# Kernel optimization log

Measured on AMD Instinct MI355X. Metric: run time of the kernel, lower is better.

The kernel has to match this reference:

```python
import jax, jax.numpy as jnp
import numpy as np

H = 512   # lstm_hidden_size
B = 64    # batch
S = 256   # seqlen


def setup_inputs() -> dict:
    key = jax.random.key(0)
    ks = jax.random.split(key, 6)
    scale = 1.0 / np.sqrt(H)  # PyTorch LSTM default init range
    return {
        "x": jax.random.normal(ks[0], (B, S, 2 * H), dtype=jnp.float32),
        "hi": jax.random.normal(ks[1], (B, S, 2 * H), dtype=jnp.float32),
        "W_ih": jax.random.uniform(ks[2], (4 * H, 5 * H), minval=-scale, maxval=scale, dtype=jnp.float32),
        "W_hh": jax.random.uniform(ks[3], (4 * H, H), minval=-scale, maxval=scale, dtype=jnp.float32),
        "b_ih": jax.random.uniform(ks[4], (4 * H,), minval=-scale, maxval=scale, dtype=jnp.float32),
        "b_hh": jax.random.uniform(ks[5], (4 * H,), minval=-scale, maxval=scale, dtype=jnp.float32),
    }


def _forward(x, hi, W_ih, W_hh, b_ih, b_hh):
    h_dim = W_hh.shape[1]
    bias = b_ih + b_hh
    xc = jnp.concatenate([x, hi], axis=-1)          # [B, S, 4H]
    xc = jnp.transpose(xc, (1, 0, 2))               # [S, B, 4H]
    batch = xc.shape[1]

    def cell(hc, inp_b):
        # inp_b: [5H]; PyTorch LSTM treats the batch dim as seq (batch_first=False quirk)
        h, c = hc
        gates = inp_b @ W_ih.T + h @ W_hh.T + bias  # [4H]
        i_g, f_g, g_g, o_g = jnp.split(gates, 4)
        i_g = jax.nn.sigmoid(i_g)
        f_g = jax.nn.sigmoid(f_g)
        g_g = jnp.tanh(g_g)
        o_g = jax.nn.sigmoid(o_g)
        c = f_g * c + i_g * g_g
        h = o_g * jnp.tanh(c)
        return (h, c), h

    def step(carry, x_i):
        out_prev, h, c = carry                      # out_prev: [B, H]
        inp = jnp.concatenate([x_i, out_prev], axis=-1)  # [B, 5H]
        (h, c), outs = jax.lax.scan(cell, (h, c), inp)    # scan over batch dim
        return (outs, h, c), outs

    init = (jnp.zeros((batch, h_dim), x.dtype),
            jnp.zeros((h_dim,), x.dtype),
            jnp.zeros((h_dim,), x.dtype))
    _, all_out = jax.lax.scan(step, init, xc)       # [S, B, H]
    return jnp.transpose(all_out, (1, 0, 2))        # [B, S, H]


def reference(x, hi, W_ih, W_hh, b_ih, b_hh):
    # Dropout layers are identity in eval mode.
    return _forward(x, hi, W_ih, W_hh, b_ih, b_hh)
```

## Files before the change

### kernel.cpp

```cpp
#include <hip/hip_runtime.h>

typedef _Float16 f16;
typedef _Float16 f16x2 __attribute__((ext_vector_type(2)));
typedef _Float16 f16x4 __attribute__((ext_vector_type(4)));
typedef _Float16 f16x8 __attribute__((ext_vector_type(8)));
typedef float f32x4 __attribute__((ext_vector_type(4)));
typedef unsigned int u32;
typedef unsigned int u32x4 __attribute__((ext_vector_type(4)));
typedef unsigned long long ull;

#define HD 512
#define T_TOT 16384
#define RING 128
#define NWG 16
#define NTH 512

static const size_t O_XC    = 0;
static const size_t O_W1    = 67108864;
static const size_t O_WHH   = 75497472;
static const size_t O_W2    = 77594624;
static const size_t O_G     = 79691776;
static const size_t O_RINGL = 213909504;
static const size_t O_RINGG = 214171648;
static const size_t O_ELECT = 214433792;

__device__ __forceinline__ float dot2f(f16x2 a, f16x2 b, float c) {
#if __has_builtin(__builtin_amdgcn_fdot2)
    return __builtin_amdgcn_fdot2(a, b, c, false);
#else
    return fmaf((float)a[0], (float)b[0], fmaf((float)a[1], (float)b[1], c));
#endif
}
__device__ __forceinline__ f16x2 bcf(u32 u) { return __builtin_bit_cast(f16x2, u); }

__device__ __forceinline__ float sigf(float x) { return 1.0f / (1.0f + __expf(-x)); }
__device__ __forceinline__ float tanhfast(float x) { return 1.0f - 2.0f / (__expf(2.0f * x) + 1.0f); }

__device__ __forceinline__ ull ld_a64(const ull* p) {
    return __hip_atomic_load(p, __ATOMIC_RELAXED, __HIP_MEMORY_SCOPE_AGENT);
}
__device__ __forceinline__ void st_a64(ull* p, ull v) {
    __hip_atomic_store(p, v, __ATOMIC_RELAXED, __HIP_MEMORY_SCOPE_AGENT);
}
__device__ __forceinline__ void ld4_sc0(const ull* p, ull& a, ull& b, ull& c, ull& d) {
    asm volatile("global_load_dwordx2 %0, %4, off sc0\n\t"
                 "global_load_dwordx2 %1, %4, off offset:8 sc0\n\t"
                 "global_load_dwordx2 %2, %4, off offset:16 sc0\n\t"
                 "global_load_dwordx2 %3, %4, off offset:24 sc0\n\t"
                 "s_waitcnt vmcnt(0)"
                 : "=&v"(a), "=&v"(b), "=&v"(c), "=&v"(d) : "v"(p) : "memory");
}
__device__ __forceinline__ void st1_sc0(ull* p, ull v) {
    asm volatile("global_store_dwordx2 %0, %1, off sc0" :: "v"(p), "v"(v) : "memory");
}

__global__ __launch_bounds__(256) void conv_xc(const float* __restrict__ x,
                                               const float* __restrict__ hi,
                                               f16* __restrict__ xc) {
    int gid = blockIdx.x * 256 + threadIdx.x;
    int t = gid >> 9;
    int k = (gid & 511) << 2;
    int b = t & 63, s = t >> 6;
    const float* src = (k < 1024) ? (x  + ((size_t)((b << 8) + s) << 10) + k)
                                  : (hi + ((size_t)((b << 8) + s) << 10) + (k - 1024));
    float4 v = *reinterpret_cast<const float4*>(src);
    f16x4 o = { (_Float16)v.x, (_Float16)v.y, (_Float16)v.z, (_Float16)v.w };
    *reinterpret_cast<f16x4*>(xc + ((size_t)t << 11) + k) = o;
}

__global__ __launch_bounds__(256) void conv_w1(const float* __restrict__ wih,
                                               f16* __restrict__ w1) {
    int gid = blockIdx.x * 256 + threadIdx.x;
    int j = gid >> 9;
    int k = (gid & 511) << 2;
    float4 v = *reinterpret_cast<const float4*>(wih + (size_t)j * 2560 + k);
    f16x4 o = { (_Float16)v.x, (_Float16)v.y, (_Float16)v.z, (_Float16)v.w };
    *reinterpret_cast<f16x4*>(w1 + ((size_t)j << 11) + k) = o;
}

__global__ __launch_bounds__(256) void conv_wc(const float* __restrict__ whh,
                                               const float* __restrict__ wih,
                                               f16* __restrict__ whhf,
                                               f16* __restrict__ w2f) {
    int gid = blockIdx.x * 256 + threadIdx.x;
    int j = gid >> 7;
    int k = (gid & 127) << 2;
    float4 a = *reinterpret_cast<const float4*>(whh + (size_t)j * 512 + k);
    f16x4 oa = { (_Float16)a.x, (_Float16)a.y, (_Float16)a.z, (_Float16)a.w };
    *reinterpret_cast<f16x4*>(whhf + ((size_t)j << 9) + k) = oa;
    float4 bv = *reinterpret_cast<const float4*>(wih + (size_t)j * 2560 + 2048 + k);
    f16x4 ob = { (_Float16)bv.x, (_Float16)bv.y, (_Float16)bv.z, (_Float16)bv.w };
    *reinterpret_cast<f16x4*>(w2f + ((size_t)j << 9) + k) = ob;
}

__global__ __launch_bounds__(256) void gemm_pre(const f16* __restrict__ XC,
                                                const f16* __restrict__ W1,
                                                const float* __restrict__ b_ih,
                                                const float* __restrict__ b_hh,
                                                float* __restrict__ G) {
    int w = threadIdx.x >> 6, l = threadIdx.x & 63;
    int R0 = blockIdx.y * 128 + (w >> 1) * 64;
    int C0 = blockIdx.x * 128 + (w & 1) * 64;
    int lr = l & 15, kb = l >> 4;
    f32x4 acc[4][4] = {};
    const f16* Abase = XC + (size_t)(R0 + lr) * 2048 + kb * 8;
    const f16* Bbase = W1 + (size_t)(C0 + lr) * 2048 + kb * 8;
    for (int kk = 0; kk < 2048; kk += 32) {
        f16x8 av[4], bv[4];
#pragma unroll
        for (int i = 0; i < 4; i++)
            av[i] = *reinterpret_cast<const f16x8*>(Abase + (size_t)(i * 16) * 2048 + kk);
#pragma unroll
        for (int i = 0; i < 4; i++)
            bv[i] = *reinterpret_cast<const f16x8*>(Bbase + (size_t)(i * 16) * 2048 + kk);
#pragma unroll
        for (int fr = 0; fr < 4; fr++)
#pragma unroll
            for (int fc = 0; fc < 4; fc++)
                acc[fr][fc] = __builtin_amdgcn_mfma_f32_16x16x32_f16(av[fr], bv[fc], acc[fr][fc], 0, 0, 0);
    }
#pragma unroll
    for (int fc = 0; fc < 4; fc++) {
        int col = C0 + fc * 16 + lr;
        float bias = b_ih[col] + b_hh[col];
#pragma unroll
        for (int fr = 0; fr < 4; fr++) {
#pragma unroll
            for (int r = 0; r < 4; r++) {
                int row = R0 + fr * 16 + kb * 4 + r;
                G[(size_t)row * 2048 + col] = acc[fr][fc][r] + bias;
            }
        }
    }
}

template <int COOP>
__global__ __launch_bounds__(NTH, 1) void lstm_chain_t(const float* __restrict__ G,
                                                       const f16* __restrict__ Whhf,
                                                       const f16* __restrict__ W2f,
                                                       ull* __restrict__ ringL,
                                                       ull* __restrict__ ringG,
                                                       int* __restrict__ elect,
                                                       float* __restrict__ out) {
    __shared__ u32 hist[96][256];
    __shared__ __align__(16) float part[2][32][4];
    __shared__ int s_slot;

    const int tid = threadIdx.x;
    int wg;
    if (COOP) {
        if (tid == 0) {
            int xcc = 0;
            asm volatile("s_getreg_b32 %0, hwreg(HW_REG_XCC_ID, 0, 32)" : "=s"(xcc));
            xcc &= 7;
            int s = atomicAdd(&elect[xcc], 1);
            if (s == 15) atomicCAS(&elect[8], 0, xcc + 1);
            int w;
            do {
                w = __hip_atomic_load(&elect[8], __ATOMIC_RELAXED, __HIP_MEMORY_SCOPE_AGENT);
            } while (w == 0);
            s_slot = (w - 1 == xcc && s < NWG) ? s : -1;
        }
        __syncthreads();
        wg = s_slot;
        if (wg < 0) return;
    } else {
        wg = blockIdx.x;
    }

    const int wv = tid >> 6, l = tid & 63;
    const int g = wv & 3, uh = (wv >> 2) & 1;
    const int rr = ((l & 1) << 3) | ((l & 2) << 1) | ((l & 4) >> 1) | ((l & 8) >> 3);
    const int row0 = g * 512 + wg * 32 + uh * 16;
    const int growD = row0 + rr;

    for (int i = tid; i < 4096; i += NTH)
        reinterpret_cast<u32x4*>(hist)[i] = (u32x4){0u, 0u, 0u, 0u};

    u32x4 w1v[16], w2v[16];
    {
        const f16* a0 = Whhf + (size_t)row0 * 512 + 8 * l;
        const f16* a1 = a0 + 4 * 512;
        const f16* a2 = a0 + 8 * 512;
        const f16* a3 = a0 + 12 * 512;
        asm volatile(
            "global_load_dwordx4 %0, %16, off\n\t"
            "global_load_dwordx4 %1, %16, off offset:1024\n\t"
            "global_load_dwordx4 %2, %16, off offset:2048\n\t"
            "global_load_dwordx4 %3, %16, off offset:3072\n\t"
            "global_load_dwordx4 %4, %17, off\n\t"
            "global_load_dwordx4 %5, %17, off offset:1024\n\t"
            "global_load_dwordx4 %6, %17, off offset:2048\n\t"
            "global_load_dwordx4 %7, %17, off offset:3072\n\t"
            "global_load_dwordx4 %8, %18, off\n\t"
            "global_load_dwordx4 %9, %18, off offset:1024\n\t"
            "global_load_dwordx4 %10, %18, off offset:2048\n\t"
            "global_load_dwordx4 %11, %18, off offset:3072\n\t"
            "global_load_dwordx4 %12, %19, off\n\t"
            "global_load_dwordx4 %13, %19, off offset:1024\n\t"
            "global_load_dwordx4 %14, %19, off offset:2048\n\t"
            "global_load_dwordx4 %15, %19, off offset:3072\n\t"
            "s_waitcnt vmcnt(0)"
            : "=&v"(w1v[0]), "=&v"(w1v[1]), "=&v"(w1v[2]), "=&v"(w1v[3]),
              "=&v"(w1v[4]), "=&v"(w1v[5]), "=&v"(w1v[6]), "=&v"(w1v[7]),
              "=&v"(w1v[8]), "=&v"(w1v[9]), "=&v"(w1v[10]), "=&v"(w1v[11]),
              "=&v"(w1v[12]), "=&v"(w1v[13]), "=&v"(w1v[14]), "=&v"(w1v[15])
            : "v"(a0), "v"(a1), "v"(a2), "v"(a3) : "memory");
        const f16* b0p = W2f + (size_t)row0 * 512 + 8 * l;
        const f16* b1p = b0p + 4 * 512;
        const f16* b2p = b0p + 8 * 512;
        const f16* b3p = b0p + 12 * 512;
        asm volatile(
            "global_load_dwordx4 %0, %16, off\n\t"
            "global_load_dwordx4 %1, %16, off offset:1024\n\t"
            "global_load_dwordx4 %2, %16, off offset:2048\n\t"
            "global_load_dwordx4 %3, %16, off offset:3072\n\t"
            "global_load_dwordx4 %4, %17, off\n\t"
            "global_load_dwordx4 %5, %17, off offset:1024\n\t"
            "global_load_dwordx4 %6, %17, off offset:2048\n\t"
            "global_load_dwordx4 %7, %17, off offset:3072\n\t"
            "global_load_dwordx4 %8, %18, off\n\t"
            "global_load_dwordx4 %9, %18, off offset:1024\n\t"
            "global_load_dwordx4 %10, %18, off offset:2048\n\t"
            "global_load_dwordx4 %11, %18, off offset:3072\n\t"
            "global_load_dwordx4 %12, %19, off\n\t"
            "global_load_dwordx4 %13, %19, off offset:1024\n\t"
            "global_load_dwordx4 %14, %19, off offset:2048\n\t"
            "global_load_dwordx4 %15, %19, off offset:3072\n\t"
            "s_waitcnt vmcnt(0)"
            : "=&v"(w2v[0]), "=&v"(w2v[1]), "=&v"(w2v[2]), "=&v"(w2v[3]),
              "=&v"(w2v[4]), "=&v"(w2v[5]), "=&v"(w2v[6]), "=&v"(w2v[7]),
              "=&v"(w2v[8]), "=&v"(w2v[9]), "=&v"(w2v[10]), "=&v"(w2v[11]),
              "=&v"(w2v[12]), "=&v"(w2v[13]), "=&v"(w2v[14]), "=&v"(w2v[15])
            : "v"(b0p), "v"(b1p), "v"(b2p), "v"(b3p) : "memory");
    }

    float cst = 0.0f;
    float gv = (l < 16) ? G[growD] : 0.0f;
    bool fb = (COOP == 0);
    __syncthreads();

    for (int t = 0; t < T_TOT; t++) {
        const int buf = t & 1;

        float ac[16];
#pragma unroll
        for (int r = 0; r < 16; r++) ac[r] = 0.0f;
        {
            u32x4 hv = *reinterpret_cast<const u32x4*>(&hist[t & 63][4 * l]);
            f16x2 h0 = bcf(hv.x), h1 = bcf(hv.y), h2 = bcf(hv.z), h3 = bcf(hv.w);
#pragma unroll
            for (int r = 0; r < 16; r++) {
                ac[r] = dot2f(bcf(w2v[r].x), h0, ac[r]);
                ac[r] = dot2f(bcf(w2v[r].y), h1, ac[r]);
                ac[r] = dot2f(bcf(w2v[r].z), h2, ac[r]);
                ac[r] = dot2f(bcf(w2v[r].w), h3, ac[r]);
            }
        }
        int tn = (t + 1 < T_TOT) ? t + 1 : t;
        float gnext = (l < 16) ? G[(size_t)tn * 2048 + growD] : 0.0f;

        u32x4 hB;
        if (wv == 0) {
            __builtin_amdgcn_s_setprio(1);
            const size_t soff = (size_t)((t - 1) & (RING - 1)) * 256 + 4 * l;
            const u32 want = (u32)t;
            ull b0 = 0, b1 = 0, b2 = 0, b3 = 0;
            bool got = false;
            if (!fb) {
                int tries = 0;
                while (!got && tries < 512) {
                    ld4_sc0(ringL + soff, b0, b1, b2, b3);
                    got = ((((u32)(b0 >> 32) ^ want) | ((u32)(b1 >> 32) ^ want) |
                            ((u32)(b2 >> 32) ^ want) | ((u32)(b3 >> 32) ^ want)) == 0u);
                    if (!got) { __builtin_amdgcn_s_sleep(1); ++tries; }
                }
                if (__any(!got)) { fb = true; got = false; }
            }
            if (!got) {
                const ull* pG = ringG + soff;
                do {
                    b0 = ld_a64(pG + 0); b1 = ld_a64(pG + 1);
                    b2 = ld_a64(pG + 2); b3 = ld_a64(pG + 3);
                } while ((((u32)(b0 >> 32) ^ want) | ((u32)(b1 >> 32) ^ want) |
                          ((u32)(b2 >> 32) ^ want) | ((u32)(b3 >> 32) ^ want)) != 0u);
            }
            hB = (u32x4){(u32)b0, (u32)b1, (u32)b2, (u32)b3};
            *reinterpret_cast<u32x4*>(&hist[(t - 1) & 63][4 * l]) = hB;
            __builtin_amdgcn_s_setprio(0);
        }
        __syncthreads();
        if (wv != 0)
            hB = *reinterpret_cast<const u32x4*>(&hist[(t - 1) & 63][4 * l]);

        {
            f16x2 h0 = bcf(hB.x), h1 = bcf(hB.y), h2 = bcf(hB.z), h3 = bcf(hB.w);
#pragma unroll
            for (int r = 0; r < 16; r++) {
                ac[r] = dot2f(bcf(w1v[r].x), h0, ac[r]);
                ac[r] = dot2f(bcf(w1v[r].y), h1, ac[r]);
                ac[r] = dot2f(bcf(w1v[r].z), h2, ac[r]);
                ac[r] = dot2f(bcf(w1v[r].w), h3, ac[r]);
            }
        }

        const bool s0 = l & 1, s1 = l & 2, s2 = l & 4, s3 = l & 8;
        float rb[8];
#pragma unroll
        for (int r = 0; r < 8; r++)
            rb[r] = (s0 ? ac[r + 8] : ac[r]) + __shfl_xor((s0 ? ac[r] : ac[r + 8]), 1);
        float rc[4];
#pragma unroll
        for (int r = 0; r < 4; r++)
            rc[r] = (s1 ? rb[r + 4] : rb[r]) + __shfl_xor((s1 ? rb[r] : rb[r + 4]), 2);
        float re[2];
#pragma unroll
        for (int r = 0; r < 2; r++)
            re[r] = (s2 ? rc[r + 2] : rc[r]) + __shfl_xor((s2 ? rc[r] : rc[r + 2]), 4);
        float d = (s3 ? re[1] : re[0]) + __shfl_xor((s3 ? re[0] : re[1]), 8);
        d += __shfl_xor(d, 16);
        d += __shfl_xor(d, 32);
        if (l < 16)
            part[buf][uh * 16 + rr][g] = d + gv;
        gv = gnext;
        __syncthreads();

        const int u = l & 31;
        float4 pg = *reinterpret_cast<const float4*>(part[buf][u]);
        float fi = sigf(pg.x), ff = sigf(pg.y);
        float fgg = tanhfast(pg.z), fo = sigf(pg.w);
        cst = ff * cst + fi * fgg;
        float h = fo * tanhfast(cst);

        u32 hb = (u32)__builtin_bit_cast(unsigned short, (f16)h);
        u32 plo = (u32)__shfl((int)hb, 2 * (l & 15));
        u32 phi = (u32)__shfl((int)hb, 2 * (l & 15) + 1);
        ull pv = (ull)(plo & 0xffffu) | ((ull)(phi & 0xffffu) << 16) |
                 ((ull)(u32)(t + 1) << 32);
        const size_t woff = (size_t)(t & (RING - 1)) * 256 + wg * 16 + (l & 15);
        if (COOP) {
            if (wv == 0 && l < 16) st1_sc0(ringL + woff, pv);
            if (wv == 2 && l < 16) st_a64(ringG + woff, pv);
        } else {
            if (wv == 0 && l < 16) st_a64(ringG + woff, pv);
        }
        if (wv == 1 && l < 32) {
            int b = t & 63, s = t >> 6;
            out[((size_t)((b << 8) + s)) * 512 + wg * 32 + l] = h;
        }
    }
}

extern "C" void kernel_launch(void* const* d_in, const int* in_sizes, int n_in,
                              void* d_out, int out_size, void* d_ws, size_t ws_size,
                              hipStream_t stream) {
    const float* x    = (const float*)d_in[0];
    const float* hi   = (const float*)d_in[1];
    const float* W_ih = (const float*)d_in[2];
    const float* W_hh = (const float*)d_in[3];
    const float* b_ih = (const float*)d_in[4];
    const float* b_hh = (const float*)d_in[5];

    char* ws = (char*)d_ws;
    f16*   XCf   = (f16*)(ws + O_XC);
    f16*   W1f   = (f16*)(ws + O_W1);
    f16*   Whhf  = (f16*)(ws + O_WHH);
    f16*   W2f   = (f16*)(ws + O_W2);
    float* G     = (float*)(ws + O_G);
    ull*   ringL = (ull*)(ws + O_RINGL);
    ull*   ringG = (ull*)(ws + O_RINGG);
    int*   elect = (int*)(ws + O_ELECT);
    float* outp  = (float*)d_out;

    hipMemsetAsync(ringL, 0, 2 * (size_t)RING * 256 * sizeof(ull) + 64, stream);

    conv_xc<<<32768, 256, 0, stream>>>(x, hi, XCf);
    conv_w1<<<4096, 256, 0, stream>>>(W_ih, W1f);
    conv_wc<<<1024, 256, 0, stream>>>(W_hh, W_ih, Whhf, W2f);
    gemm_pre<<<dim3(16, 128), 256, 0, stream>>>(XCf, W1f, b_ih, b_hh, G);

    const f16* cWhhf = Whhf;
    const f16* cW2f  = W2f;
    const float* cG  = G;
    void* kargs[] = { (void*)&cG, (void*)&cWhhf, (void*)&cW2f,
                      (void*)&ringL, (void*)&ringG, (void*)&elect, (void*)&outp };
    hipError_t e = hipLaunchCooperativeKernel((const void*)lstm_chain_t<1>,
                                              dim3(256), dim3(NTH), kargs, 0, stream);
    if (e != hipSuccess) {
        lstm_chain_t<0><<<NWG, NTH, 0, stream>>>(G, Whhf, W2f, ringL, ringG, elect, outp);
    }
}
```

Baseline: 31.30 ms.

## Add helper wavefront for gate-input prefetch, global ring stores, and output writes

Adds a ninth wavefront that prefetches precomputed input-gate values two steps ahead into a shared double buffer and handles the global ring store and output write. Compute waves no longer load G in the critical loop, and only waves 0 and 8 run the cell update. The local-ring spin drops s_sleep and raises the retry limit. The aim is to take global memory traffic off the serial recurrence path. The cost is an extra wave per block and busier polling that may contend with other traffic.

Result: slower. 48.67 ms (+55.5%).

```diff
diff --git a/kernel.cpp b/kernel.cpp
--- a/kernel.cpp
+++ b/kernel.cpp
@@ -13,7 +13,7 @@
 #define T_TOT 16384
 #define RING 128
 #define NWG 16
-#define NTH 512
+#define NTH 576
 
 static const size_t O_XC    = 0;
 static const size_t O_W1    = 67108864;
@@ -144,6 +144,7 @@
                                                        float* __restrict__ out) {
     __shared__ u32 hist[96][256];
     __shared__ __align__(16) float part[2][32][4];
+    __shared__ __align__(16) float gbuf[2][32][4];
     __shared__ int s_slot;
 
     const int tid = threadIdx.x;
@@ -172,7 +173,6 @@
     const int g = wv & 3, uh = (wv >> 2) & 1;
     const int rr = ((l & 1) << 3) | ((l & 2) << 1) | ((l & 4) >> 1) | ((l & 8) >> 3);
     const int row0 = g * 512 + wg * 32 + uh * 16;
-    const int growD = row0 + rr;
 
     for (int i = tid; i < 4096; i += NTH)
         reinterpret_cast<u32x4*>(hist)[i] = (u32x4){0u, 0u, 0u, 0u};
@@ -235,8 +235,19 @@
             : "v"(b0p), "v"(b1p), "v"(b2p), "v"(b3p) : "memory");
     }
 
+    float4 gv4 = {0.f, 0.f, 0.f, 0.f};
+    if (wv == 8 && l < 32) {
+        float4 g0;
+#pragma unroll
+        for (int g2 = 0; g2 < 4; g2++)
+            ((float*)&g0)[g2] = G[(size_t)g2 * 512 + wg * 32 + l];
+        *reinterpret_cast<float4*>(&gbuf[0][l][0]) = g0;
+#pragma unroll
+        for (int g2 = 0; g2 < 4; g2++)
+            ((float*)&gv4)[g2] = G[(size_t)2048 + g2 * 512 + wg * 32 + l];
+    }
+
     float cst = 0.0f;
-    float gv = (l < 16) ? G[growD] : 0.0f;
     bool fb = (COOP == 0);
     __syncthreads();
 
@@ -246,7 +257,8 @@
         float ac[16];
 #pragma unroll
         for (int r = 0; r < 16; r++) ac[r] = 0.0f;
-        {
+
+        if (wv < 8) {
             u32x4 hv = *reinterpret_cast<const u32x4*>(&hist[t & 63][4 * l]);
             f16x2 h0 = bcf(hv.x), h1 = bcf(hv.y), h2 = bcf(hv.z), h3 = bcf(hv.w);
 #pragma unroll
@@ -257,8 +269,6 @@
                 ac[r] = dot2f(bcf(w2v[r].w), h3, ac[r]);
             }
         }
-        int tn = (t + 1 < T_TOT) ? t + 1 : t;
-        float gnext = (l < 16) ? G[(size_t)tn * 2048 + growD] : 0.0f;
 
         u32x4 hB;
         if (wv == 0) {
@@ -269,11 +279,11 @@
             bool got = false;
             if (!fb) {
                 int tries = 0;
-                while (!got && tries < 512) {
+                while (!got && tries < 8192) {
                     ld4_sc0(ringL + soff, b0, b1, b2, b3);
                     got = ((((u32)(b0 >> 32) ^ want) | ((u32)(b1 >> 32) ^ want) |
                             ((u32)(b2 >> 32) ^ want) | ((u32)(b3 >> 32) ^ want)) == 0u);
-                    if (!got) { __builtin_amdgcn_s_sleep(1); ++tries; }
+                    ++tries;
                 }
                 if (__any(!got)) { fb = true; got = false; }
             }
@@ -288,65 +298,72 @@
             hB = (u32x4){(u32)b0, (u32)b1, (u32)b2, (u32)b3};
             *reinterpret_cast<u32x4*>(&hist[(t - 1) & 63][4 * l]) = hB;
             __builtin_amdgcn_s_setprio(0);
+        } else if (wv == 8) {
+            if (l < 32) {
+                *reinterpret_cast<float4*>(&gbuf[buf ^ 1][l][0]) = gv4;
+                int tf = (t + 2 < T_TOT) ? t + 2 : T_TOT - 1;
+#pragma unroll
+                for (int g2 = 0; g2 < 4; g2++)
+                    ((float*)&gv4)[g2] = G[(size_t)tf * 2048 + g2 * 512 + wg * 32 + l];
+            }
         }
         __syncthreads();
-        if (wv != 0)
-            hB = *reinterpret_cast<const u32x4*>(&hist[(t - 1) & 63][4 * l]);
-
-        {
-            f16x2 h0 = bcf(hB.x), h1 = bcf(hB.y), h2 = bcf(hB.z), h3 = bcf(hB.w);
-#pragma unroll
-            for (int r = 0; r < 16; r++) {
-                ac[r] = dot2f(bcf(w1v[r].x), h0, ac[r]);
-                ac[r] = dot2f(bcf(w1v[r].y), h1, ac[r]);
-                ac[r] = dot2f(bcf(w1v[r].z), h2, ac[r]);
-                ac[r] = dot2f(bcf(w1v[r].w), h3, ac[r]);
-            }
-        }
-
-        const bool s0 = l & 1, s1 = l & 2, s2 = l & 4, s3 = l & 8;
-        float rb[8];
-#pragma unroll
-        for (int r = 0; r < 8; r++)
-            rb[r] = (s0 ? ac[r + 8] : ac[r]) + __shfl_xor((s0 ? ac[r] : ac[r + 8]), 1);
-        float rc[4];
-#pragma unroll
-        for (int r = 0; r < 4; r++)
-            rc[r] = (s1 ? rb[r + 4] : rb[r]) + __shfl_xor((s1 ? rb[r] : rb[r + 4]), 2);
-        float re[2];
-#pragma unroll
-        for (int r = 0; r < 2; r++)
-            re[r] = (s2 ? rc[r + 2] : rc[r]) + __shfl_xor((s2 ? rc[r] : rc[r + 2]), 4);
-        float d = (s3 ? re[1] : re[0]) + __shfl_xor((s3 ? re[0] : re[1]), 8);
-        d += __shfl_xor(d, 16);
-        d += __shfl_xor(d, 32);
-        if (l < 16)
-            part[buf][uh * 16 + rr][g] = d + gv;
-        gv = gnext;
+
+        if (wv < 8) {
+            if (wv != 0)
+                hB = *reinterpret_cast<const u32x4*>(&hist[(t - 1) & 63][4 * l]);
+            {
+                f16x2 h0 = bcf(hB.x), h1 = bcf(hB.y), h2 = bcf(hB.z), h3 = bcf(hB.w);
+#pragma unroll
+                for (int r = 0; r < 16; r++) {
+                    ac[r] = dot2f(bcf(w1v[r].x), h0, ac[r]);
+                    ac[r] = dot2f(bcf(w1v[r].y), h1, ac[r]);
+                    ac[r] = dot2f(bcf(w1v[r].z), h2, ac[r]);
+                    ac[r] = dot2f(bcf(w1v[r].w), h3, ac[r]);
+                }
+            }
+            const bool s0 = l & 1, s1 = l & 2, s2 = l & 4, s3 = l & 8;
+            float rb[8];
+#pragma unroll
+            for (int r = 0; r < 8; r++)
+                rb[r] = (s0 ? ac[r + 8] : ac[r]) + __shfl_xor((s0 ? ac[r] : ac[r + 8]), 1);
+            float rc[4];
+#pragma unroll
+            for (int r = 0; r < 4; r++)
+                rc[r] = (s1 ? rb[r + 4] : rb[r]) + __shfl_xor((s1 ? rb[r] : rb[r + 4]), 2);
+            float re[2];
+#pragma unroll
+            for (int r = 0; r < 2; r++)
+                re[r] = (s2 ? rc[r + 2] : rc[r]) + __shfl_xor((s2 ? rc[r] : rc[r + 2]), 4);
+            float d = (s3 ? re[1] : re[0]) + __shfl_xor((s3 ? re[0] : re[1]), 8);
+            d += __shfl_xor(d, 16);
+            d += __shfl_xor(d, 32);
+            if (l < 16)
+                part[buf][uh * 16 + rr][g] = d;
+        }
         __syncthreads();
 
-        const int u = l & 31;
-        float4 pg = *reinterpret_cast<const float4*>(part[buf][u]);
-        float fi = sigf(pg.x), ff = sigf(pg.y);
-        float fgg = tanhfast(pg.z), fo = sigf(pg.w);
-        cst = ff * cst + fi * fgg;
-        float h = fo * tanhfast(cst);
-
-        u32 hb = (u32)__builtin_bit_cast(unsigned short, (f16)h);
-        u32 plo = (u32)__shfl((int)hb, 2 * (l & 15));
-        u32 phi = (u32)__shfl((int)hb, 2 * (l & 15) + 1);
-        ull pv = (ull)(plo & 0xffffu) | ((ull)(phi & 0xffffu) << 16) |
-                 ((ull)(u32)(t + 1) << 32);
-        const size_t woff = (size_t)(t & (RING - 1)) * 256 + wg * 16 + (l & 15);
-        if (COOP) {
-            if (wv == 0 && l < 16) st1_sc0(ringL + woff, pv);
-            if (wv == 2 && l < 16) st_a64(ringG + woff, pv);
-        } else {
-            if (wv == 0 && l < 16) st_a64(ringG + woff, pv);
-        }
-        if (wv == 1 && l < 32) {
-            int b = t & 63, s = t >> 6;
-            out[((size_t)((b << 8) + s)) * 512 + wg * 32 + l] = h;
+        if (wv == 0 || wv == 8) {
+            const int u = l & 31;
+            float4 pg = *reinterpret_cast<const float4*>(part[buf][u]);
+            float4 gb = *reinterpret_cast<const float4*>(&gbuf[buf][u][0]);
+            float fi = sigf(pg.x + gb.x), ff = sigf(pg.y + gb.y);
+            float fgg = tanhfast(pg.z + gb.z), fo = sigf(pg.w + gb.w);
+            cst = ff * cst + fi * fgg;
+            float h = fo * tanhfast(cst);
+
+            u32 hb = (u32)__builtin_bit_cast(unsigned short, (f16)h);
+            u32 plo = (u32)__shfl((int)hb, 2 * (l & 15));
+            u32 phi = (u32)__shfl((int)hb, 2 * (l & 15) + 1);
+            ull pv = (ull)(plo & 0xffffu) | ((ull)(phi & 0xffffu) << 16) |
+                     ((ull)(u32)(t + 1) << 32);
+            const size_t woff = (size_t)(t & (RING - 1)) * 256 + wg * 16 + (l & 15);
+            if (COOP && wv == 0 && l < 16) st1_sc0(ringL + woff, pv);
+            if (wv == 8 && l < 16) st_a64(ringG + woff, pv);
+            if (wv == 8 && l < 32) {
+                int b = t & 63, s = t >> 6;
+                out[((size_t)((b << 8) + s)) * 512 + wg * 32 + l] = h;
+            }
         }
     }
 }
```
